# Optimization experiments

Measured on AMD Instinct MI355X. Metric: run time of the kernel, lower is better.

Reference implementation:

```python
import jax, jax.numpy as jnp
import numpy as np

N = 50000
E = 800000
D_IN = 128
D_H = 128
D_OUT = 57
NEG_SLOPE = 0.2


def setup_inputs() -> dict:
    key = jax.random.key(0)
    ks = jax.random.split(key, 12)
    s_in = 1.0 / np.sqrt(D_IN)
    s_h = 1.0 / np.sqrt(D_H)
    return {
        "x": jax.random.normal(ks[0], (N, D_IN), jnp.float32),
        "edge_index": jax.random.randint(ks[1], (2, E), 0, N, jnp.int64),
        "W1": jax.random.normal(ks[2], (D_IN, D_H), jnp.float32) * s_in,
        "a1_src": jax.random.normal(ks[3], (D_H,), jnp.float32) * s_h,
        "a1_dst": jax.random.normal(ks[4], (D_H,), jnp.float32) * s_h,
        "b1": jnp.zeros((D_H,), jnp.float32),
        "W2": jax.random.normal(ks[5], (D_H, D_H), jnp.float32) * s_h,
        "a2_src": jax.random.normal(ks[6], (D_H,), jnp.float32) * s_h,
        "a2_dst": jax.random.normal(ks[7], (D_H,), jnp.float32) * s_h,
        "b2": jnp.zeros((D_H,), jnp.float32),
        "fc_w": jax.random.normal(ks[8], (D_H, D_OUT), jnp.float32) * s_h,
        "fc_b": jnp.zeros((D_OUT,), jnp.float32),
    }


def _gat_layer(x, src, dst, n, W, a_src, a_dst, b):
    """Single-head PyG GATConv (concat=True, heads=1). src/dst include self-loops."""
    h = x @ W                                # [N, Dh]
    alpha_s = h @ a_src                      # [N]
    alpha_d = h @ a_dst                      # [N]
    e = alpha_s[src] + alpha_d[dst]          # [E+N] per-edge logit
    e = jnp.where(e > 0, e, NEG_SLOPE * e)   # leaky_relu
    # segment softmax over incoming edges of each destination node
    m = jax.ops.segment_max(e, dst, num_segments=n)
    m = jnp.where(jnp.isfinite(m), m, 0.0)
    ex = jnp.exp(e - m[dst])
    den = jax.ops.segment_sum(ex, dst, num_segments=n)
    w = ex / den[dst]                        # [E+N] attention weights
    out = jax.ops.segment_sum(w[:, None] * h[src], dst, num_segments=n)
    return out + b


def reference(x, edge_index, W1, a1_src, a1_dst, b1, W2, a2_src, a2_dst, b2, fc_w, fc_b):
    n = x.shape[0]
    loops = jnp.arange(n, dtype=edge_index.dtype)
    src = jnp.concatenate([edge_index[0], loops])
    dst = jnp.concatenate([edge_index[1], loops])
    h = jax.nn.relu(_gat_layer(x, src, dst, n, W1, a1_src, a1_dst, b1))
    # dropout p=0.5 is identity in eval mode
    h = _gat_layer(h, src, dst, n, W2, a2_src, a2_dst, b2)
    return h @ fc_w + fc_b
```

## Files before the change

kernel.cpp:

```cpp
#include <hip/hip_runtime.h>
#include <hip/hip_fp16.h>


#define NEG_SLOPE 0.2f

struct __align__(8) half4_t { __half2 a, b; };

__global__ void probe_i64_kernel(const int* __restrict__ ei, int E, int* __restrict__ flag)
{
    int lane = threadIdx.x;
    int v = 0;
    int lim = (E < 256) ? E : 256;
    for (int t = lane; t < lim; t += 64) v |= ei[2 * t + 1];
    #pragma unroll
    for (int o = 32; o >= 1; o >>= 1) v |= __shfl_xor(v, o);
    if (lane == 0) flag[0] = (v == 0) ? 1 : 0;
}

__global__ __launch_bounds__(256) void count_deg_kernel(
    const int* __restrict__ ei, int E, int n,
    const int* __restrict__ flag, int* __restrict__ deg)
{
    int is64 = flag[0];
    int half = (E + 1) >> 1;
    int i2 = blockIdx.x * blockDim.x + threadIdx.x;
    if (i2 >= half) return;
    int e0 = 2 * i2;
    bool has1 = (e0 + 1) < E;
    int d0, d1 = 0;
    if (is64) {
        const int2* p = (const int2*)ei;
        d0 = p[E + e0].x;
        if (has1) d1 = p[E + e0 + 1].x;
    } else {
        d0 = ei[E + e0];
        if (has1) d1 = ei[E + e0 + 1];
    }
    atomicAdd(&deg[d0], 1);
    if (has1) atomicAdd(&deg[d1], 1);
}

__global__ __launch_bounds__(1024) void scan1_kernel(
    const int* __restrict__ deg, int* __restrict__ rowptr,
    int* __restrict__ csum, int n)
{
    __shared__ int wsum[16];
    int b = blockIdx.x, tid = threadIdx.x;
    int lane = tid & 63, wv = tid >> 6;
    int i = b * 1024 + tid;
    int v = (i < n) ? (deg[i] + 1) : 0;
    int s = v;
    #pragma unroll
    for (int off = 1; off < 64; off <<= 1) {
        int t = __shfl_up(s, off);
        if (lane >= off) s += t;
    }
    if (lane == 63) wsum[wv] = s;
    __syncthreads();
    if (wv == 0) {
        int ws = (lane < 16) ? wsum[lane] : 0;
        #pragma unroll
        for (int off = 1; off < 16; off <<= 1) {
            int t = __shfl_up(ws, off);
            if (lane >= off) ws += t;
        }
        if (lane < 16) wsum[lane] = ws;
    }
    __syncthreads();
    int woff = (wv == 0) ? 0 : wsum[wv - 1];
    int incl = woff + s;
    if (i < n) rowptr[i + 1] = incl;
    if (tid == 1023) csum[b] = incl;
    if (b == 0 && tid == 0) rowptr[0] = 0;
}

__global__ void scan2_kernel(int* __restrict__ csum, int nb)
{
    int lane = threadIdx.x;
    int v = (lane < nb) ? csum[lane] : 0;
    #pragma unroll
    for (int off = 1; off < 64; off <<= 1) {
        int t = __shfl_up(v, off);
        if (lane >= off) v += t;
    }
    if (lane < nb) csum[lane] = v;
}

__global__ __launch_bounds__(1024) void scan3_kernel(
    const int* __restrict__ csum, int* __restrict__ rowptr, int n)
{
    int b = blockIdx.x + 1;
    int i = b * 1024 + threadIdx.x;
    if (i < n) rowptr[i + 1] += csum[b - 1];
}

__global__ __launch_bounds__(256) void scatter_kernel(
    const int* __restrict__ ei, int E, int n,
    const int* __restrict__ flag,
    const int* __restrict__ rowptr, int* __restrict__ deg, int* __restrict__ col)
{
    int is64 = flag[0];
    int half = (E + 1) >> 1;
    int i2 = blockIdx.x * blockDim.x + threadIdx.x;
    if (i2 < half) {
        int e0 = 2 * i2;
        bool has1 = (e0 + 1) < E;
        int s0, d0, s1 = 0, d1 = 0;
        if (is64) {
            const int2* p = (const int2*)ei;
            s0 = p[e0].x;     d0 = p[E + e0].x;
            if (has1) { s1 = p[e0 + 1].x; d1 = p[E + e0 + 1].x; }
        } else {
            s0 = ei[e0];      d0 = ei[E + e0];
            if (has1) { s1 = ei[e0 + 1];  d1 = ei[E + e0 + 1]; }
        }
        int pos0 = atomicSub(&deg[d0], 1) - 1;
        col[rowptr[d0] + pos0] = s0;
        if (has1) {
            int pos1 = atomicSub(&deg[d1], 1) - 1;
            col[rowptr[d1] + pos1] = s1;
        }
    } else {
        int d = i2 - half;
        if (d < n) col[rowptr[d + 1] - 1] = d;
    }
}

__global__ __launch_bounds__(256) void gemm_h_kernel(
    const float* __restrict__ X, const float* __restrict__ W,
    const float* __restrict__ asv, const float* __restrict__ adv,
    __half* __restrict__ H16, float* __restrict__ As, float* __restrict__ Ad, int n)
{
    __shared__ float Wl[64 * 128];
    int tid = threadIdx.x;
    int cg = tid & 15, rg = tid >> 4;
    int row0 = blockIdx.x * 32;
    int r0 = row0 + rg * 2, r1 = r0 + 1;
    int rc0 = (r0 < n) ? r0 : (n - 1);
    int rc1 = (r1 < n) ? r1 : (n - 1);

    float acc[2][8];
    #pragma unroll
    for (int i = 0; i < 2; ++i)
        #pragma unroll
        for (int c = 0; c < 8; ++c) acc[i][c] = 0.f;

    const float4* Wl4 = (const float4*)Wl;

    #pragma unroll
    for (int p = 0; p < 2; ++p) {
        {
            const float4* W4 = (const float4*)(W + p * 64 * 128);
            float4* Wl4w = (float4*)Wl;
            #pragma unroll
            for (int t = 0; t < 8; ++t) Wl4w[tid + t * 256] = W4[tid + t * 256];
        }
        __syncthreads();

        const float* X0 = X + (size_t)rc0 * 128 + p * 64;
        const float* X1 = X + (size_t)rc1 * 128 + p * 64;
        for (int k = 0; k < 64; k += 4) {
            float4 xa = *(const float4*)(X0 + k);
            float4 xb = *(const float4*)(X1 + k);
            #pragma unroll
            for (int kk = 0; kk < 4; ++kk) {
                float4 wA = Wl4[(k + kk) * 32 + cg];
                float4 wB = Wl4[(k + kk) * 32 + 16 + cg];
                float x0s = (kk == 0) ? xa.x : (kk == 1) ? xa.y : (kk == 2) ? xa.z : xa.w;
                float x1s = (kk == 0) ? xb.x : (kk == 1) ? xb.y : (kk == 2) ? xb.z : xb.w;
                acc[0][0] += x0s * wA.x; acc[0][1] += x0s * wA.y;
                acc[0][2] += x0s * wA.z; acc[0][3] += x0s * wA.w;
                acc[0][4] += x0s * wB.x; acc[0][5] += x0s * wB.y;
                acc[0][6] += x0s * wB.z; acc[0][7] += x0s * wB.w;
                acc[1][0] += x1s * wA.x; acc[1][1] += x1s * wA.y;
                acc[1][2] += x1s * wA.z; acc[1][3] += x1s * wA.w;
                acc[1][4] += x1s * wB.x; acc[1][5] += x1s * wB.y;
                acc[1][6] += x1s * wB.z; acc[1][7] += x1s * wB.w;
            }
        }
        __syncthreads();
    }

    float4 asA = *(const float4*)(asv + cg * 4);
    float4 asB = *(const float4*)(asv + 64 + cg * 4);
    float4 adA = *(const float4*)(adv + cg * 4);
    float4 adB = *(const float4*)(adv + 64 + cg * 4);

    #pragma unroll
    for (int i = 0; i < 2; ++i) {
        int r = r0 + i;
        float ps = acc[i][0] * asA.x + acc[i][1] * asA.y + acc[i][2] * asA.z + acc[i][3] * asA.w
                 + acc[i][4] * asB.x + acc[i][5] * asB.y + acc[i][6] * asB.z + acc[i][7] * asB.w;
        float pd = acc[i][0] * adA.x + acc[i][1] * adA.y + acc[i][2] * adA.z + acc[i][3] * adA.w
                 + acc[i][4] * adB.x + acc[i][5] * adB.y + acc[i][6] * adB.z + acc[i][7] * adB.w;
        #pragma unroll
        for (int mask = 8; mask >= 1; mask >>= 1) {
            ps += __shfl_xor(ps, mask);
            pd += __shfl_xor(pd, mask);
        }
        if (r < n) {
            half4_t hlo, hhi;
            hlo.a = __floats2half2_rn(acc[i][0], acc[i][1]);
            hlo.b = __floats2half2_rn(acc[i][2], acc[i][3]);
            hhi.a = __floats2half2_rn(acc[i][4], acc[i][5]);
            hhi.b = __floats2half2_rn(acc[i][6], acc[i][7]);
            *(half4_t*)(H16 + (size_t)r * 128 + cg * 4)      = hlo;
            *(half4_t*)(H16 + (size_t)r * 128 + 64 + cg * 4) = hhi;
            if (cg == 0) { As[r] = ps; Ad[r] = pd; }
        }
    }
}

__global__ __launch_bounds__(256) void gat_agg_kernel(
    const __half* __restrict__ H16, const float* __restrict__ As, const float* __restrict__ Ad,
    const int* __restrict__ rowptr, const int* __restrict__ col,
    const float* __restrict__ bias, float* __restrict__ Out, int n, int relu)
{
    int wid = (blockIdx.x * blockDim.x + threadIdx.x) >> 6;
    int lane = threadIdx.x & 63;
    if (wid >= n) return;

    int beg = rowptr[wid], end = rowptr[wid + 1];
    int degn = end - beg;
    float adn = Ad[wid];

    int c0r = 0;
    if (lane < degn) c0r = col[beg + lane];

    float ex0 = 0.f;
    if (lane < degn) {
        float e = As[c0r] + adn;
        e = (e > 0.f) ? e : NEG_SLOPE * e;
        ex0 = __expf(e);
    }
    float den = ex0;
    for (int j = beg + lane + 64; j < end; j += 64) {
        float e = As[col[j]] + adn;
        e = (e > 0.f) ? e : NEG_SLOPE * e;
        den += __expf(e);
    }
    #pragma unroll
    for (int o = 32; o >= 1; o >>= 1) den += __shfl_xor(den, o);
    float inv = 1.f / den;

    const __half2* H2 = (const __half2*)H16;
    float accx = 0.f, accy = 0.f;
    int nfull = (degn < 64) ? degn : 64;
    int j = 0;
    for (; j + 8 <= nfull; j += 8) {
        int ss[8]; float ww[8]; __half2 hh[8];
        #pragma unroll
        for (int u = 0; u < 8; ++u) { ss[u] = __shfl(c0r, j + u); ww[u] = __shfl(ex0, j + u); }
        #pragma unroll
        for (int u = 0; u < 8; ++u) { hh[u] = H2[(size_t)ss[u] * 64 + lane]; }
        #pragma unroll
        for (int u = 0; u < 8; ++u) {
            float2 f = __half22float2(hh[u]);
            accx += ww[u] * f.x; accy += ww[u] * f.y;
        }
    }
    for (; j < nfull; ++j) {
        int s = __shfl(c0r, j);
        float w = __shfl(ex0, j);
        float2 f = __half22float2(H2[(size_t)s * 64 + lane]);
        accx += w * f.x; accy += w * f.y;
    }
    for (int jj = 64; jj < degn; ++jj) {
        int s = col[beg + jj];
        float e = As[s] + adn;
        e = (e > 0.f) ? e : NEG_SLOPE * e;
        float w = __expf(e);
        float2 f = __half22float2(H2[(size_t)s * 64 + lane]);
        accx += w * f.x; accy += w * f.y;
    }

    float2 b2 = ((const float2*)bias)[lane];
    float ox = accx * inv + b2.x;
    float oy = accy * inv + b2.y;
    if (relu) { ox = fmaxf(ox, 0.f); oy = fmaxf(oy, 0.f); }
    float2 o2; o2.x = ox; o2.y = oy;
    ((float2*)Out)[(size_t)wid * 64 + lane] = o2;
}

__global__ __launch_bounds__(256) void fc_kernel(
    const float* __restrict__ H, const float* __restrict__ Wf,
    const float* __restrict__ bf, float* __restrict__ Out, int n)
{
    __shared__ float Wl[128 * 64];
    int tid = threadIdx.x;
    for (int i = tid; i < 128 * 64; i += 256) {
        int k = i >> 6, c = i & 63;
        Wl[i] = (c < 57) ? Wf[k * 57 + c] : 0.f;
    }
    __syncthreads();

    int cg = tid & 15, rg = tid >> 4;
    int c0 = cg * 4;
    int row0 = blockIdx.x * 32;
    int r0 = row0 + rg * 2, r1 = r0 + 1;
    int rc0 = (r0 < n) ? r0 : (n - 1);
    int rc1 = (r1 < n) ? r1 : (n - 1);

    float acc[2][4];
    #pragma unroll
    for (int i = 0; i < 2; ++i)
        #pragma unroll
        for (int c = 0; c < 4; ++c) acc[i][c] = 0.f;

    const float* X0 = H + (size_t)rc0 * 128;
    const float* X1 = H + (size_t)rc1 * 128;
    const float4* Wl4 = (const float4*)Wl;

    for (int k = 0; k < 128; k += 4) {
        float4 xa = *(const float4*)(X0 + k);
        float4 xb = *(const float4*)(X1 + k);
        #pragma unroll
        for (int kk = 0; kk < 4; ++kk) {
            float4 wv = Wl4[(k + kk) * 16 + cg];
            float x0s = (kk == 0) ? xa.x : (kk == 1) ? xa.y : (kk == 2) ? xa.z : xa.w;
            float x1s = (kk == 0) ? xb.x : (kk == 1) ? xb.y : (kk == 2) ? xb.z : xb.w;
            acc[0][0] += x0s * wv.x; acc[0][1] += x0s * wv.y;
            acc[0][2] += x0s * wv.z; acc[0][3] += x0s * wv.w;
            acc[1][0] += x1s * wv.x; acc[1][1] += x1s * wv.y;
            acc[1][2] += x1s * wv.z; acc[1][3] += x1s * wv.w;
        }
    }

    #pragma unroll
    for (int i = 0; i < 2; ++i) {
        int r = r0 + i;
        if (r >= n) continue;
        #pragma unroll
        for (int cc = 0; cc < 4; ++cc) {
            int c = c0 + cc;
            if (c < 57) Out[(size_t)r * 57 + c] = acc[i][cc] + bf[c];
        }
    }
}


extern "C" void kernel_launch(void* const* d_in, const int* in_sizes, int n_in,
                              void* d_out, int out_size, void* d_ws, size_t ws_size,
                              hipStream_t stream)
{
    const float* x   = (const float*)d_in[0];
    const int*   ei  = (const int*)d_in[1];
    const float* W1  = (const float*)d_in[2];
    const float* a1s = (const float*)d_in[3];
    const float* a1d = (const float*)d_in[4];
    const float* b1  = (const float*)d_in[5];
    const float* W2  = (const float*)d_in[6];
    const float* a2s = (const float*)d_in[7];
    const float* a2d = (const float*)d_in[8];
    const float* b2  = (const float*)d_in[9];
    const float* fcw = (const float*)d_in[10];
    const float* fcb = (const float*)d_in[11];
    float* out = (float*)d_out;

    int n = in_sizes[0] / 128;
    int E = in_sizes[1] / 2;
    int tot = E + n;
    int nchunks = (n + 1023) / 1024;
    int half = (E + 1) >> 1;

    char* ws = (char*)d_ws;
    size_t off = 0;
    auto alloc = [&](size_t bytes) -> void* {
        void* p = ws + off;
        off += (bytes + 255) & ~(size_t)255;
        return p;
    };
    __half* h16   = (__half*)alloc((size_t)n * 128 * 2);
    float* hF     = (float*)alloc((size_t)n * 128 * 4);
    float* As     = (float*)alloc((size_t)n * 4);
    float* Ad     = (float*)alloc((size_t)n * 4);
    int*   rowptr = (int*)alloc((size_t)(n + 1) * 4);
    int*   deg    = (int*)alloc((size_t)n * 4);
    int*   col    = (int*)alloc((size_t)tot * 4);
    int*   flag   = (int*)alloc(256);
    int*   csum   = (int*)alloc((size_t)64 * 4);

    hipMemsetAsync(deg, 0, (size_t)n * 4, stream);

    probe_i64_kernel<<<1, 64, 0, stream>>>(ei, E, flag);

    int cb = (half + 255) / 256;
    count_deg_kernel<<<cb, 256, 0, stream>>>(ei, E, n, flag, deg);
    scan1_kernel<<<nchunks, 1024, 0, stream>>>(deg, rowptr, csum, n);
    scan2_kernel<<<1, 64, 0, stream>>>(csum, nchunks);
    if (nchunks > 1)
        scan3_kernel<<<nchunks - 1, 1024, 0, stream>>>(csum, rowptr, n);
    int sb = (half + n + 255) / 256;
    scatter_kernel<<<sb, 256, 0, stream>>>(ei, E, n, flag, rowptr, deg, col);

    int gb = (n + 31) / 32;
    int ab = (n + 3) / 4;

    gemm_h_kernel<<<gb, 256, 0, stream>>>(x, W1, a1s, a1d, h16, As, Ad, n);
    gat_agg_kernel<<<ab, 256, 0, stream>>>(h16, As, Ad, rowptr, col, b1, hF, n, 1);
    gemm_h_kernel<<<gb, 256, 0, stream>>>(hF, W2, a2s, a2d, h16, As, Ad, n);
    gat_agg_kernel<<<ab, 256, 0, stream>>>(h16, As, Ad, rowptr, col, b2, hF, n, 0);
    fc_kernel<<<gb, 256, 0, stream>>>(hF, fcw, fcb, out, n);
}
```

Baseline: 353.6 us.

## Fuse degree counting into first GEMM launch and process four edges per thread

Merges the degree-count pass and the layer-1 feature GEMM into one launch: the leading blocks do the atomic degree counts and the remaining blocks compute X@W1, so the two independent jobs overlap on the GPU. The count and scatter kernels now handle four edges per thread with int4 vector loads instead of two scalar loads. The change saves one launch and the serialization between counting and the GEMM. In exchange, early-exiting count blocks share a kernel with the GEMM blocks' shared-memory footprint, and the int4 loads assume aligned edge arrays.

New measurement: 336.8 us. 4.8% less time.

```diff
diff --git a/kernel.cpp b/kernel.cpp
--- a/kernel.cpp
+++ b/kernel.cpp
@@ -17,124 +17,46 @@
     if (lane == 0) flag[0] = (v == 0) ? 1 : 0;
 }
 
-__global__ __launch_bounds__(256) void count_deg_kernel(
+__global__ __launch_bounds__(256) void fused_count_gemm_kernel(
     const int* __restrict__ ei, int E, int n,
-    const int* __restrict__ flag, int* __restrict__ deg)
-{
-    int is64 = flag[0];
-    int half = (E + 1) >> 1;
-    int i2 = blockIdx.x * blockDim.x + threadIdx.x;
-    if (i2 >= half) return;
-    int e0 = 2 * i2;
-    bool has1 = (e0 + 1) < E;
-    int d0, d1 = 0;
-    if (is64) {
-        const int2* p = (const int2*)ei;
-        d0 = p[E + e0].x;
-        if (has1) d1 = p[E + e0 + 1].x;
-    } else {
-        d0 = ei[E + e0];
-        if (has1) d1 = ei[E + e0 + 1];
-    }
-    atomicAdd(&deg[d0], 1);
-    if (has1) atomicAdd(&deg[d1], 1);
-}
-
-__global__ __launch_bounds__(1024) void scan1_kernel(
-    const int* __restrict__ deg, int* __restrict__ rowptr,
-    int* __restrict__ csum, int n)
-{
-    __shared__ int wsum[16];
-    int b = blockIdx.x, tid = threadIdx.x;
-    int lane = tid & 63, wv = tid >> 6;
-    int i = b * 1024 + tid;
-    int v = (i < n) ? (deg[i] + 1) : 0;
-    int s = v;
-    #pragma unroll
-    for (int off = 1; off < 64; off <<= 1) {
-        int t = __shfl_up(s, off);
-        if (lane >= off) s += t;
-    }
-    if (lane == 63) wsum[wv] = s;
-    __syncthreads();
-    if (wv == 0) {
-        int ws = (lane < 16) ? wsum[lane] : 0;
-        #pragma unroll
-        for (int off = 1; off < 16; off <<= 1) {
-            int t = __shfl_up(ws, off);
-            if (lane >= off) ws += t;
-        }
-        if (lane < 16) wsum[lane] = ws;
-    }
-    __syncthreads();
-    int woff = (wv == 0) ? 0 : wsum[wv - 1];
-    int incl = woff + s;
-    if (i < n) rowptr[i + 1] = incl;
-    if (tid == 1023) csum[b] = incl;
-    if (b == 0 && tid == 0) rowptr[0] = 0;
-}
-
-__global__ void scan2_kernel(int* __restrict__ csum, int nb)
-{
-    int lane = threadIdx.x;
-    int v = (lane < nb) ? csum[lane] : 0;
-    #pragma unroll
-    for (int off = 1; off < 64; off <<= 1) {
-        int t = __shfl_up(v, off);
-        if (lane >= off) v += t;
-    }
-    if (lane < nb) csum[lane] = v;
-}
-
-__global__ __launch_bounds__(1024) void scan3_kernel(
-    const int* __restrict__ csum, int* __restrict__ rowptr, int n)
-{
-    int b = blockIdx.x + 1;
-    int i = b * 1024 + threadIdx.x;
-    if (i < n) rowptr[i + 1] += csum[b - 1];
-}
-
-__global__ __launch_bounds__(256) void scatter_kernel(
-    const int* __restrict__ ei, int E, int n,
-    const int* __restrict__ flag,
-    const int* __restrict__ rowptr, int* __restrict__ deg, int* __restrict__ col)
-{
-    int is64 = flag[0];
-    int half = (E + 1) >> 1;
-    int i2 = blockIdx.x * blockDim.x + threadIdx.x;
-    if (i2 < half) {
-        int e0 = 2 * i2;
-        bool has1 = (e0 + 1) < E;
-        int s0, d0, s1 = 0, d1 = 0;
-        if (is64) {
-            const int2* p = (const int2*)ei;
-            s0 = p[e0].x;     d0 = p[E + e0].x;
-            if (has1) { s1 = p[e0 + 1].x; d1 = p[E + e0 + 1].x; }
-        } else {
-            s0 = ei[e0];      d0 = ei[E + e0];
-            if (has1) { s1 = ei[e0 + 1];  d1 = ei[E + e0 + 1]; }
-        }
-        int pos0 = atomicSub(&deg[d0], 1) - 1;
-        col[rowptr[d0] + pos0] = s0;
-        if (has1) {
-            int pos1 = atomicSub(&deg[d1], 1) - 1;
-            col[rowptr[d1] + pos1] = s1;
-        }
-    } else {
-        int d = i2 - half;
-        if (d < n) col[rowptr[d + 1] - 1] = d;
-    }
-}
-
-__global__ __launch_bounds__(256) void gemm_h_kernel(
+    const int* __restrict__ flag, int* __restrict__ deg, int cntBlocks,
     const float* __restrict__ X, const float* __restrict__ W,
     const float* __restrict__ asv, const float* __restrict__ adv,
-    __half* __restrict__ H16, float* __restrict__ As, float* __restrict__ Ad, int n)
+    __half* __restrict__ H16, float* __restrict__ As, float* __restrict__ Ad)
 {
     __shared__ float Wl[64 * 128];
+
+    if ((int)blockIdx.x < cntBlocks) {
+        int is64 = flag[0];
+        int base = (blockIdx.x * 256 + threadIdx.x) * 4;
+        if (base >= E) return;
+        int d[4];
+        int cnt;
+        if (base + 4 <= E) {
+            cnt = 4;
+            if (is64) {
+                const int4* q = (const int4*)ei;
+                int4 a = q[(E + base) >> 1];
+                int4 b = q[((E + base) >> 1) + 1];
+                d[0] = a.x; d[1] = a.z; d[2] = b.x; d[3] = b.z;
+            } else {
+                int4 a = *(const int4*)(ei + E + base);
+                d[0] = a.x; d[1] = a.y; d[2] = a.z; d[3] = a.w;
+            }
+        } else {
+            cnt = E - base;
+            for (int u = 0; u < cnt; ++u)
+                d[u] = is64 ? ei[2 * (E + base + u)] : ei[E + base + u];
+        }
+        #pragma unroll
+        for (int u = 0; u < 4; ++u)
+            if (u < cnt) atomicAdd(&deg[d[u]], 1);
+        return;
+    }
+
     int tid = threadIdx.x;
     int cg = tid & 15, rg = tid >> 4;
-    int row0 = blockIdx.x * 32;
+    int row0 = ((int)blockIdx.x - cntBlocks) * 32;
     int r0 = row0 + rg * 2, r1 = r0 + 1;
     int rc0 = (r0 < n) ? r0 : (n - 1);
     int rc1 = (r1 < n) ? r1 : (n - 1);
@@ -211,6 +133,193 @@
     }
 }
 
+__global__ __launch_bounds__(1024) void scan1_kernel(
+    const int* __restrict__ deg, int* __restrict__ rowptr,
+    int* __restrict__ csum, int n)
+{
+    __shared__ int wsum[16];
+    int b = blockIdx.x, tid = threadIdx.x;
+    int lane = tid & 63, wv = tid >> 6;
+    int i = b * 1024 + tid;
+    int v = (i < n) ? (deg[i] + 1) : 0;
+    int s = v;
+    #pragma unroll
+    for (int off = 1; off < 64; off <<= 1) {
+        int t = __shfl_up(s, off);
+        if (lane >= off) s += t;
+    }
+    if (lane == 63) wsum[wv] = s;
+    __syncthreads();
+    if (wv == 0) {
+        int ws = (lane < 16) ? wsum[lane] : 0;
+        #pragma unroll
+        for (int off = 1; off < 16; off <<= 1) {
+            int t = __shfl_up(ws, off);
+            if (lane >= off) ws += t;
+        }
+        if (lane < 16) wsum[lane] = ws;
+    }
+    __syncthreads();
+    int woff = (wv == 0) ? 0 : wsum[wv - 1];
+    int incl = woff + s;
+    if (i < n) rowptr[i + 1] = incl;
+    if (tid == 1023) csum[b] = incl;
+    if (b == 0 && tid == 0) rowptr[0] = 0;
+}
+
+__global__ void scan2_kernel(int* __restrict__ csum, int nb)
+{
+    int lane = threadIdx.x;
+    int v = (lane < nb) ? csum[lane] : 0;
+    #pragma unroll
+    for (int off = 1; off < 64; off <<= 1) {
+        int t = __shfl_up(v, off);
+        if (lane >= off) v += t;
+    }
+    if (lane < nb) csum[lane] = v;
+}
+
+__global__ __launch_bounds__(1024) void scan3_kernel(
+    const int* __restrict__ csum, int* __restrict__ rowptr, int n)
+{
+    int b = blockIdx.x + 1;
+    int i = b * 1024 + threadIdx.x;
+    if (i < n) rowptr[i + 1] += csum[b - 1];
+}
+
+__global__ __launch_bounds__(256) void scatter_kernel(
+    const int* __restrict__ ei, int E, int n,
+    const int* __restrict__ flag,
+    const int* __restrict__ rowptr, int* __restrict__ deg, int* __restrict__ col)
+{
+    int is64 = flag[0];
+    int quarter = (E + 3) >> 2;
+    int iq = blockIdx.x * blockDim.x + threadIdx.x;
+    if (iq < quarter) {
+        int base = iq * 4;
+        int s[4], d[4];
+        int cnt;
+        if (base + 4 <= E) {
+            cnt = 4;
+            if (is64) {
+                const int4* q = (const int4*)ei;
+                int4 sa = q[base >> 1];
+                int4 sb = q[(base >> 1) + 1];
+                int4 da = q[(E + base) >> 1];
+                int4 db = q[((E + base) >> 1) + 1];
+                s[0] = sa.x; s[1] = sa.z; s[2] = sb.x; s[3] = sb.z;
+                d[0] = da.x; d[1] = da.z; d[2] = db.x; d[3] = db.z;
+            } else {
+                int4 sa = *(const int4*)(ei + base);
+                int4 da = *(const int4*)(ei + E + base);
+                s[0] = sa.x; s[1] = sa.y; s[2] = sa.z; s[3] = sa.w;
+                d[0] = da.x; d[1] = da.y; d[2] = da.z; d[3] = da.w;
+            }
+        } else {
+            cnt = E - base;
+            for (int u = 0; u < cnt; ++u) {
+                if (is64) { s[u] = ei[2 * (base + u)]; d[u] = ei[2 * (E + base + u)]; }
+                else      { s[u] = ei[base + u];       d[u] = ei[E + base + u]; }
+            }
+        }
+        #pragma unroll
+        for (int u = 0; u < 4; ++u) {
+            if (u < cnt) {
+                int pos = atomicSub(&deg[d[u]], 1) - 1;
+                col[rowptr[d[u]] + pos] = s[u];
+            }
+        }
+    } else {
+        int dd = iq - quarter;
+        if (dd < n) col[rowptr[dd + 1] - 1] = dd;
+    }
+}
+
+__global__ __launch_bounds__(256) void gemm_h_kernel(
+    const float* __restrict__ X, const float* __restrict__ W,
+    const float* __restrict__ asv, const float* __restrict__ adv,
+    __half* __restrict__ H16, float* __restrict__ As, float* __restrict__ Ad, int n)
+{
+    __shared__ float Wl[64 * 128];
+    int tid = threadIdx.x;
+    int cg = tid & 15, rg = tid >> 4;
+    int row0 = blockIdx.x * 32;
+    int r0 = row0 + rg * 2, r1 = r0 + 1;
+    int rc0 = (r0 < n) ? r0 : (n - 1);
+    int rc1 = (r1 < n) ? r1 : (n - 1);
+
+    float acc[2][8];
+    #pragma unroll
+    for (int i = 0; i < 2; ++i)
+        #pragma unroll
+        for (int c = 0; c < 8; ++c) acc[i][c] = 0.f;
+
+    const float4* Wl4 = (const float4*)Wl;
+
+    #pragma unroll
+    for (int p = 0; p < 2; ++p) {
+        {
+            const float4* W4 = (const float4*)(W + p * 64 * 128);
+            float4* Wl4w = (float4*)Wl;
+            #pragma unroll
+            for (int t = 0; t < 8; ++t) Wl4w[tid + t * 256] = W4[tid + t * 256];
+        }
+        __syncthreads();
+
+        const float* X0 = X + (size_t)rc0 * 128 + p * 64;
+        const float* X1 = X + (size_t)rc1 * 128 + p * 64;
+        for (int k = 0; k < 64; k += 4) {
+            float4 xa = *(const float4*)(X0 + k);
+            float4 xb = *(const float4*)(X1 + k);
+            #pragma unroll
+            for (int kk = 0; kk < 4; ++kk) {
+                float4 wA = Wl4[(k + kk) * 32 + cg];
+                float4 wB = Wl4[(k + kk) * 32 + 16 + cg];
+                float x0s = (kk == 0) ? xa.x : (kk == 1) ? xa.y : (kk == 2) ? xa.z : xa.w;
+                float x1s = (kk == 0) ? xb.x : (kk == 1) ? xb.y : (kk == 2) ? xb.z : xb.w;
+                acc[0][0] += x0s * wA.x; acc[0][1] += x0s * wA.y;
+                acc[0][2] += x0s * wA.z; acc[0][3] += x0s * wA.w;
+                acc[0][4] += x0s * wB.x; acc[0][5] += x0s * wB.y;
+                acc[0][6] += x0s * wB.z; acc[0][7] += x0s * wB.w;
+                acc[1][0] += x1s * wA.x; acc[1][1] += x1s * wA.y;
+                acc[1][2] += x1s * wA.z; acc[1][3] += x1s * wA.w;
+                acc[1][4] += x1s * wB.x; acc[1][5] += x1s * wB.y;
+                acc[1][6] += x1s * wB.z; acc[1][7] += x1s * wB.w;
+            }
+        }
+        __syncthreads();
+    }
+
+    float4 asA = *(const float4*)(asv + cg * 4);
+    float4 asB = *(const float4*)(asv + 64 + cg * 4);
+    float4 adA = *(const float4*)(adv + cg * 4);
+    float4 adB = *(const float4*)(adv + 64 + cg * 4);
+
+    #pragma unroll
+    for (int i = 0; i < 2; ++i) {
+        int r = r0 + i;
+        float ps = acc[i][0] * asA.x + acc[i][1] * asA.y + acc[i][2] * asA.z + acc[i][3] * asA.w
+                 + acc[i][4] * asB.x + acc[i][5] * asB.y + acc[i][6] * asB.z + acc[i][7] * asB.w;
+        float pd = acc[i][0] * adA.x + acc[i][1] * adA.y + acc[i][2] * adA.z + acc[i][3] * adA.w
+                 + acc[i][4] * adB.x + acc[i][5] * adB.y + acc[i][6] * adB.z + acc[i][7] * adB.w;
+        #pragma unroll
+        for (int mask = 8; mask >= 1; mask >>= 1) {
+            ps += __shfl_xor(ps, mask);
+            pd += __shfl_xor(pd, mask);
+        }
+        if (r < n) {
+            half4_t hlo, hhi;
+            hlo.a = __floats2half2_rn(acc[i][0], acc[i][1]);
+            hlo.b = __floats2half2_rn(acc[i][2], acc[i][3]);
+            hhi.a = __floats2half2_rn(acc[i][4], acc[i][5]);
+            hhi.b = __floats2half2_rn(acc[i][6], acc[i][7]);
+            *(half4_t*)(H16 + (size_t)r * 128 + cg * 4)      = hlo;
+            *(half4_t*)(H16 + (size_t)r * 128 + 64 + cg * 4) = hhi;
+            if (cg == 0) { As[r] = ps; Ad[r] = pd; }
+        }
+    }
+}
+
 __global__ __launch_bounds__(256) void gat_agg_kernel(
     const __half* __restrict__ H16, const float* __restrict__ As, const float* __restrict__ Ad,
     const int* __restrict__ rowptr, const int* __restrict__ col,
@@ -361,7 +470,7 @@
     int E = in_sizes[1] / 2;
     int tot = E + n;
     int nchunks = (n + 1023) / 1024;
-    int half = (E + 1) >> 1;
+    int quarter = (E + 3) >> 2;
 
     char* ws = (char*)d_ws;
     size_t off = 0;
@@ -384,19 +493,22 @@
 
     probe_i64_kernel<<<1, 64, 0, stream>>>(ei, E, flag);
 
-    int cb = (half + 255) / 256;
-    count_deg_kernel<<<cb, 256, 0, stream>>>(ei, E, n, flag, deg);
+    int gb = (n + 31) / 32;
+    int cntBlocks = (quarter + 255) / 256;
+
+    fused_count_gemm_kernel<<<cntBlocks + gb, 256, 0, stream>>>(
+        ei, E, n, flag, deg, cntBlocks, x, W1, a1s, a1d, h16, As, Ad);
+
     scan1_kernel<<<nchunks, 1024, 0, stream>>>(deg, rowptr, csum, n);
     scan2_kernel<<<1, 64, 0, stream>>>(csum, nchunks);
     if (nchunks > 1)
         scan3_kernel<<<nchunks - 1, 1024, 0, stream>>>(csum, rowptr, n);
-    int sb = (half + n + 255) / 256;
+
+    int sb = (quarter + n + 255) / 256;
     scatter_kernel<<<sb, 256, 0, stream>>>(ei, E, n, flag, rowptr, deg, col);
 
-    int gb = (n + 31) / 32;
     int ab = (n + 3) / 4;
 
-    gemm_h_kernel<<<gb, 256, 0, stream>>>(x, W1, a1s, a1d, h16, As, Ad, n);
     gat_agg_kernel<<<ab, 256, 0, stream>>>(h16, As, Ad, rowptr, col, b1, hF, n, 1);
     gemm_h_kernel<<<gb, 256, 0, stream>>>(hF, W2, a2s, a2d, h16, As, Ad, n);
     gat_agg_kernel<<<ab, 256, 0, stream>>>(h16, As, Ad, rowptr, col, b2, hF, n, 0);
```
